# Kernel optimization log

Measured on AMD Instinct MI355X. Metric: run time of the kernel, lower is better.

## Reference

```python
import jax, jax.numpy as jnp
import numpy as np

B, N, C, H = 4, 1024, 1024, 16
HD = C // H
SCALE = HD ** -0.5


def _init_linear(key, out_dim, in_dim):
    # torch nn.Linear default init: U(-1/sqrt(in), 1/sqrt(in)) for weight and bias
    kw, kb = jax.random.split(key)
    bound = 1.0 / np.sqrt(in_dim)
    W = jax.random.uniform(kw, (out_dim, in_dim), jnp.float32, -bound, bound)
    b = jax.random.uniform(kb, (out_dim,), jnp.float32, -bound, bound)
    return W, b


def setup_inputs() -> dict:
    key = jax.random.key(0)
    ks = jax.random.split(key, 5)
    x = jax.random.normal(ks[0], (B, N, C), jnp.float32)
    # NdLinear qkv: Linear(N->N) along seq axis, then Linear(C->3C) along channel axis
    Wq0, bq0 = _init_linear(ks[1], N, N)
    Wq1, bq1 = _init_linear(ks[2], 3 * C, C)
    # NdLinear proj: Linear(N->N) along seq axis, then Linear(C->C) along channel axis
    Wp0, bp0 = _init_linear(ks[3], N, N)
    Wp1, bp1 = _init_linear(ks[4], C, C)
    return {"x": x, "Wq0": Wq0, "bq0": bq0, "Wq1": Wq1, "bq1": bq1,
            "Wp0": Wp0, "bp0": bp0, "Wp1": Wp1, "bp1": bp1}


def _ndlinear(x, W0, b0, W1, b1):
    # NdLinear over (seq, channel): apply Linear along axis 1, then axis 2.
    # torch Linear: y = x @ W.T + b
    x = jnp.einsum('bnc,mn->bmc', x, W0) + b0[None, :, None]   # seq axis
    x = jnp.einsum('bnc,dc->bnd', x, W1) + b1                  # channel axis
    return x


def reference(x, Wq0, bq0, Wq1, bq1, Wp0, bp0, Wp1, bp1):
    qkv = _ndlinear(x, Wq0, bq0, Wq1, bq1)                     # (B, N, 3C)
    qkv = qkv.reshape(B, N, 3, H, HD).transpose(2, 0, 3, 1, 4) # (3, B, H, N, HD)
    q, k, v = qkv[0], qkv[1], qkv[2]
    attn = jnp.einsum('bhnd,bhmd->bhnm', q, k) * SCALE         # (B, H, N, N)
    attn = jax.nn.softmax(attn, axis=-1)
    out = jnp.einsum('bhnm,bhmd->bhnd', attn, v)               # (B, H, N, HD)
    out = out.transpose(0, 2, 1, 3).reshape(B, N, C)
    out = _ndlinear(out, Wp0, bp0, Wp1, bp1)
    return out
```

## Files before the change

kernel.cpp:

```cpp
#include <hip/hip_runtime.h>
#include <hip/hip_bf16.h>
#include <stdint.h>

typedef __bf16 bf16;
typedef __bf16 bf16x4 __attribute__((ext_vector_type(4)));
typedef __bf16 bf16x8 __attribute__((ext_vector_type(8)));
typedef float f32x4 __attribute__((ext_vector_type(4)));

#define B_ 4
#define N_ 1024
#define C_ 1024
#define H_ 16
#define MEG (1u << 20)

__device__ __forceinline__ uint32_t lds_off(const void* p) {
    return (uint32_t)(uintptr_t)p;
}
__device__ __forceinline__ void g2l16(const void* g, uint32_t lds_byte) {
    __builtin_amdgcn_global_load_lds(
        (const __attribute__((address_space(1))) unsigned int*)(uintptr_t)g,
        (__attribute__((address_space(3))) unsigned int*)(uintptr_t)lds_byte,
        16, 0, 0);
}

__global__ __launch_bounds__(256) void cvt_k(const float* __restrict__ in,
                                             bf16* __restrict__ out, int n) {
    int i = (blockIdx.x * 256 + threadIdx.x) * 8;
    if (i >= n) return;
    float4 a = *(const float4*)(in + i);
    float4 b = *(const float4*)(in + i + 4);
    bf16x8 r;
    r[0] = (bf16)a.x; r[1] = (bf16)a.y; r[2] = (bf16)a.z; r[3] = (bf16)a.w;
    r[4] = (bf16)b.x; r[5] = (bf16)b.y; r[6] = (bf16)b.z; r[7] = (bf16)b.w;
    *(bf16x8*)(out + i) = r;
}

__global__ __launch_bounds__(256) void xpose_k(const float* __restrict__ x,
                                               bf16* __restrict__ xT) {
    __shared__ bf16 t[64][66];
    const int tid = threadIdx.x;
    const int b = blockIdx.z, n0 = blockIdx.y * 64, c0 = blockIdx.x * 64;
    {
        int nl = tid >> 2, seg = tid & 3;
        const float* src = x + ((size_t)b * N_ + n0 + nl) * C_ + c0 + seg * 16;
#pragma unroll
        for (int i = 0; i < 4; ++i) {
            float4 v = *(const float4*)(src + i * 4);
            t[nl][seg * 16 + i * 4 + 0] = (bf16)v.x;
            t[nl][seg * 16 + i * 4 + 1] = (bf16)v.y;
            t[nl][seg * 16 + i * 4 + 2] = (bf16)v.z;
            t[nl][seg * 16 + i * 4 + 3] = (bf16)v.w;
        }
    }
    __syncthreads();
    {
        int cl = tid >> 2, seg = tid & 3;
        bf16* dst = xT + ((size_t)b * C_ + c0 + cl) * N_ + n0 + seg * 16;
        bf16x8 o0, o1;
#pragma unroll
        for (int j = 0; j < 8; ++j) o0[j] = t[seg * 16 + j][cl];
#pragma unroll
        for (int j = 0; j < 8; ++j) o1[j] = t[seg * 16 + 8 + j][cl];
        *(bf16x8*)dst = o0;
        *(bf16x8*)(dst + 8) = o1;
    }
}

template <int BIAS, bool OF32>
__global__ __launch_bounds__(512) void gemm_k(
    const bf16* __restrict__ A, const bf16* __restrict__ Bm,
    const float* __restrict__ bias, void* __restrict__ Cv,
    int M, int Nn, int K, long long sA, long long sB, long long sC)
{
    __shared__ bf16 smem[2][2][128 * 64];

    const int tid = threadIdx.x;
    const int lane = tid & 63, wid = tid >> 6;
    const int lr = lane & 15, lg = lane >> 4;
    const int wr = wid >> 2, wc = wid & 3;
    const int m0 = blockIdx.y * 128, n0 = blockIdx.x * 128;

    const bf16* Ab = A + (size_t)blockIdx.z * sA;
    const bf16* Bb = Bm + (size_t)blockIdx.z * sB;

    const uint32_t a_lds0 = lds_off(&smem[0][0][0]);
    const uint32_t b_lds0 = lds_off(&smem[0][1][0]);
    const uint32_t bufstride = 2 * 128 * 64 * 2;

    auto stage = [&](int kt, int buf) {
#pragma unroll
        for (int half = 0; half < 2; ++half) {
            int it = tid + half * 512;
            int r = it >> 3, ch = it & 7;
            int sch = ch ^ (r & 7);
            g2l16(Ab + (size_t)(m0 + r) * K + kt * 64 + sch * 8,
                  a_lds0 + buf * bufstride + it * 16);
            g2l16(Bb + (size_t)(n0 + r) * K + kt * 64 + sch * 8,
                  b_lds0 + buf * bufstride + it * 16);
        }
    };

    f32x4 acc[4][2];
#pragma unroll
    for (int i = 0; i < 4; ++i)
#pragma unroll
        for (int j = 0; j < 2; ++j) { f32x4 z = {0.f,0.f,0.f,0.f}; acc[i][j] = z; }

    stage(0, 0);
    __syncthreads();

    const int nt = K >> 6;
    for (int t = 0; t < nt; ++t) {
        int buf = t & 1;
        if (t + 1 < nt) stage(t + 1, buf ^ 1);
        const bf16* As = &smem[buf][0][0];
        const bf16* Bs = &smem[buf][1][0];
#pragma unroll
        for (int s = 0; s < 2; ++s) {
            bf16x8 af[4], bfr[2];
#pragma unroll
            for (int mi = 0; mi < 4; ++mi) {
                int row = wr * 64 + mi * 16 + lr;
                int slot = (s * 4 + lg) ^ (row & 7);
                af[mi] = *(const bf16x8*)(As + row * 64 + slot * 8);
            }
#pragma unroll
            for (int ni = 0; ni < 2; ++ni) {
                int row = wc * 32 + ni * 16 + lr;
                int slot = (s * 4 + lg) ^ (row & 7);
                bfr[ni] = *(const bf16x8*)(Bs + row * 64 + slot * 8);
            }
#pragma unroll
            for (int mi = 0; mi < 4; ++mi)
#pragma unroll
                for (int ni = 0; ni < 2; ++ni)
                    acc[mi][ni] = __builtin_amdgcn_mfma_f32_16x16x32_bf16(
                        af[mi], bfr[ni], acc[mi][ni], 0, 0, 0);
        }
        __syncthreads();
    }

#pragma unroll
    for (int mi = 0; mi < 4; ++mi)
#pragma unroll
        for (int ni = 0; ni < 2; ++ni)
#pragma unroll
            for (int r = 0; r < 4; ++r) {
                int row = m0 + wr * 64 + mi * 16 + lg * 4 + r;
                int col = n0 + wc * 32 + ni * 16 + lr;
                float bv = (BIAS == 0) ? bias[row] : bias[col];
                float v = acc[mi][ni][r] + bv;
                if constexpr (OF32)
                    ((float*)Cv + (size_t)blockIdx.z * sC)[(size_t)row * Nn + col] = v;
                else
                    ((bf16*)Cv + (size_t)blockIdx.z * sC)[(size_t)row * Nn + col] = (bf16)v;
            }
}

__global__ __launch_bounds__(512) void attn_k(
    const bf16* __restrict__ qkv, bf16* __restrict__ aoT)
{
    __shared__ bf16 Ks[2][4096];
    __shared__ bf16 Vs[2][64][72];
    __shared__ bf16 pbuf[8][16][72];

    const int tid = threadIdx.x;
    const int lane = tid & 63, wid = tid >> 6;
    const int lr = lane & 15, lg = lane >> 4;
    const int bid = blockIdx.x;
    const int qt = bid >> 6, hb = bid & 63;
    const int b = hb >> 4, h = hb & 15;
    const int qrow0 = qt * 128 + wid * 16;
    const int hoff = h * 64;
    const bf16* qkvb = qkv + (size_t)b * (N_ * 3 * C_);

    bf16x8 qf[2];
#pragma unroll
    for (int kk = 0; kk < 2; ++kk)
        qf[kk] = *(const bf16x8*)(qkvb + (size_t)(qrow0 + lr) * 3072 +
                                  hoff + kk * 32 + lg * 8);

    const uint32_t ks0 = lds_off(&Ks[0][0]);
    const int vkey = tid >> 3, vdc = tid & 7;

    auto stageK = [&](int kt, int buf) {
        int key = tid >> 3, ch = tid & 7;
        int sch = ch ^ (key & 7);
        g2l16(qkvb + (size_t)(kt * 64 + key) * 3072 + C_ + hoff + sch * 8,
              ks0 + buf * 8192 + tid * 16);
    };
    auto loadV = [&](int kt) -> bf16x8 {
        return *(const bf16x8*)(qkvb + (size_t)(kt * 64 + vkey) * 3072 +
                                2 * C_ + hoff + vdc * 8);
    };
    auto writeV = [&](bf16x8 v, int buf) {
#pragma unroll
        for (int j = 0; j < 8; ++j) Vs[buf][vdc * 8 + j][vkey] = v[j];
    };

    float lsum[4] = {0.f, 0.f, 0.f, 0.f};
    f32x4 o[4];
#pragma unroll
    for (int i = 0; i < 4; ++i) { f32x4 z = {0.f,0.f,0.f,0.f}; o[i] = z; }

    stageK(0, 0);
    writeV(loadV(0), 0);
    __syncthreads();

    for (int kt = 0; kt < 16; ++kt) {
        int buf = kt & 1;
        bf16x8 vnext;
        if (kt + 1 < 16) {
            stageK(kt + 1, buf ^ 1);
            vnext = loadV(kt + 1);
        }

        f32x4 s[4];
#pragma unroll
        for (int st = 0; st < 4; ++st) {
            f32x4 z = {0.f, 0.f, 0.f, 0.f};
#pragma unroll
            for (int kk = 0; kk < 2; ++kk) {
                int row = st * 16 + lr;
                int slot = (kk * 4 + lg) ^ (row & 7);
                bf16x8 kf = *(const bf16x8*)(&Ks[buf][row * 64 + slot * 8]);
                z = __builtin_amdgcn_mfma_f32_16x16x32_bf16(qf[kk], kf, z, 0, 0, 0);
            }
            s[st] = z;
        }

#pragma unroll
        for (int st = 0; st < 4; ++st)
#pragma unroll
            for (int r = 0; r < 4; ++r) {
                float e = __expf(s[st][r] * 0.125f);
                bf16 pb = (bf16)e;
                lsum[r] += (float)pb;
                pbuf[wid][lg * 4 + r][st * 16 + lr] = pb;
            }

        bf16x8 pf[2];
        pf[0] = *(const bf16x8*)(&pbuf[wid][lr][lg * 8]);
        pf[1] = *(const bf16x8*)(&pbuf[wid][lr][32 + lg * 8]);

#pragma unroll
        for (int dt = 0; dt < 4; ++dt) {
            bf16x8 v0 = *(const bf16x8*)(&Vs[buf][dt * 16 + lr][lg * 8]);
            bf16x8 v1 = *(const bf16x8*)(&Vs[buf][dt * 16 + lr][32 + lg * 8]);
            o[dt] = __builtin_amdgcn_mfma_f32_16x16x32_bf16(pf[0], v0, o[dt], 0, 0, 0);
            o[dt] = __builtin_amdgcn_mfma_f32_16x16x32_bf16(pf[1], v1, o[dt], 0, 0, 0);
        }

        if (kt + 1 < 16) writeV(vnext, buf ^ 1);
        __syncthreads();
    }

#pragma unroll
    for (int m = 1; m < 16; m <<= 1)
#pragma unroll
        for (int r = 0; r < 4; ++r)
            lsum[r] += __shfl_xor(lsum[r], m, 64);

#pragma unroll
    for (int dt = 0; dt < 4; ++dt) {
        bf16x4 ov;
#pragma unroll
        for (int r = 0; r < 4; ++r) ov[r] = (bf16)(o[dt][r] / lsum[r]);
        size_t c = (size_t)b * C_ + hoff + dt * 16 + lr;
        *(bf16x4*)(aoT + c * N_ + qrow0 + lg * 4) = ov;
    }
}

extern "C" void kernel_launch(void* const* d_in, const int* in_sizes, int n_in,
                              void* d_out, int out_size, void* d_ws, size_t ws_size,
                              hipStream_t stream) {
    (void)in_sizes; (void)n_in; (void)out_size; (void)ws_size;
    const float* x   = (const float*)d_in[0];
    const float* Wq0 = (const float*)d_in[1];
    const float* bq0 = (const float*)d_in[2];
    const float* Wq1 = (const float*)d_in[3];
    const float* bq1 = (const float*)d_in[4];
    const float* Wp0 = (const float*)d_in[5];
    const float* bp0 = (const float*)d_in[6];
    const float* Wp1 = (const float*)d_in[7];
    const float* bp1 = (const float*)d_in[8];

    bf16* ws   = (bf16*)d_ws;
    bf16* xT   = ws;
    bf16* Wq0b = ws + 4 * MEG;
    bf16* Wq1b = ws + 5 * MEG;
    bf16* Wp0b = ws + 8 * MEG;
    bf16* Wp1b = ws + 9 * MEG;
    bf16* y1   = ws + 10 * MEG;
    bf16* y2   = ws + 14 * MEG;
    bf16* aoT  = y1;
    bf16* z1   = y2;
    float* outp = (float*)d_out;

    const long long s1M = (long long)N_ * C_;

    cvt_k<<<dim3(512), 256, 0, stream>>>(Wq0, Wq0b, 1 * MEG);
    cvt_k<<<dim3(1536), 256, 0, stream>>>(Wq1, Wq1b, 3 * MEG);
    cvt_k<<<dim3(512), 256, 0, stream>>>(Wp0, Wp0b, 1 * MEG);
    cvt_k<<<dim3(512), 256, 0, stream>>>(Wp1, Wp1b, 1 * MEG);
    xpose_k<<<dim3(16, 16, 4), 256, 0, stream>>>(x, xT);

    gemm_k<0, false><<<dim3(8, 8, 4), 512, 0, stream>>>(
        Wq0b, xT, bq0, y1, 1024, 1024, 1024, 0LL, s1M, s1M);
    gemm_k<1, false><<<dim3(24, 32, 1), 512, 0, stream>>>(
        y1, Wq1b, bq1, y2, 4096, 3072, 1024, 0LL, 0LL, 0LL);
    attn_k<<<dim3(512), 512, 0, stream>>>(y2, aoT);
    gemm_k<0, false><<<dim3(8, 8, 4), 512, 0, stream>>>(
        Wp0b, aoT, bp0, z1, 1024, 1024, 1024, 0LL, s1M, s1M);
    gemm_k<1, true><<<dim3(8, 32, 1), 512, 0, stream>>>(
        z1, Wp1b, bp1, outp, 4096, 1024, 1024, 0LL, 0LL, 0LL);
}
```

Before: 141.0 us.

## Merge weight conversion launches and swizzle transposed V tile in attention LDS

Combines the four fp32-to-bf16 weight conversion launches into a single kernel that selects its source by block index, cutting launch overhead. In the attention kernel, V is now transposed as it is gathered from global memory: each thread reads one dimension across 8 keys with strided scalar loads. It then writes a single 16-byte XOR-swizzled vector into a packed 64x64 LDS tile, replacing eight bank-conflicting scalar LDS stores per thread. The trade-off is less coalesced global loads for V, since there are 8 strided 2-byte reads per thread instead of one 16-byte read.

```diff
diff --git a/kernel.cpp b/kernel.cpp
--- a/kernel.cpp
+++ b/kernel.cpp
@@ -23,16 +23,24 @@
         16, 0, 0);
 }
 
-__global__ __launch_bounds__(256) void cvt_k(const float* __restrict__ in,
-                                             bf16* __restrict__ out, int n) {
-    int i = (blockIdx.x * 256 + threadIdx.x) * 8;
-    if (i >= n) return;
-    float4 a = *(const float4*)(in + i);
-    float4 b = *(const float4*)(in + i + 4);
+__global__ __launch_bounds__(256) void cvt4_k(
+    const float* __restrict__ s0, bf16* __restrict__ d0,
+    const float* __restrict__ s1, bf16* __restrict__ d1,
+    const float* __restrict__ s2, bf16* __restrict__ d2,
+    const float* __restrict__ s3, bf16* __restrict__ d3) {
+    int bid = blockIdx.x;
+    const float* s; bf16* d; int base;
+    if (bid < 512)       { s = s0; d = d0; base = 0; }
+    else if (bid < 2048) { s = s1; d = d1; base = 512; }
+    else if (bid < 2560) { s = s2; d = d2; base = 2048; }
+    else                 { s = s3; d = d3; base = 2560; }
+    int i = ((bid - base) * 256 + threadIdx.x) * 8;
+    float4 a = *(const float4*)(s + i);
+    float4 b = *(const float4*)(s + i + 4);
     bf16x8 r;
     r[0] = (bf16)a.x; r[1] = (bf16)a.y; r[2] = (bf16)a.z; r[3] = (bf16)a.w;
     r[4] = (bf16)b.x; r[5] = (bf16)b.y; r[6] = (bf16)b.z; r[7] = (bf16)b.w;
-    *(bf16x8*)(out + i) = r;
+    *(bf16x8*)(d + i) = r;
 }
 
 __global__ __launch_bounds__(256) void xpose_k(const float* __restrict__ x,
@@ -161,7 +169,7 @@
     const bf16* __restrict__ qkv, bf16* __restrict__ aoT)
 {
     __shared__ bf16 Ks[2][4096];
-    __shared__ bf16 Vs[2][64][72];
+    __shared__ bf16 Vs[2][4096];
     __shared__ bf16 pbuf[8][16][72];
 
     const int tid = threadIdx.x;
@@ -181,7 +189,7 @@
                                   hoff + kk * 32 + lg * 8);
 
     const uint32_t ks0 = lds_off(&Ks[0][0]);
-    const int vkey = tid >> 3, vdc = tid & 7;
+    const int vd = tid & 63, vkg = tid >> 6;
 
     auto stageK = [&](int kt, int buf) {
         int key = tid >> 3, ch = tid & 7;
@@ -190,12 +198,15 @@
               ks0 + buf * 8192 + tid * 16);
     };
     auto loadV = [&](int kt) -> bf16x8 {
-        return *(const bf16x8*)(qkvb + (size_t)(kt * 64 + vkey) * 3072 +
-                                2 * C_ + hoff + vdc * 8);
+        const bf16* base = qkvb + 2 * C_ + hoff + vd;
+        bf16x8 v;
+#pragma unroll
+        for (int j = 0; j < 8; ++j)
+            v[j] = base[(size_t)(kt * 64 + vkg * 8 + j) * 3072];
+        return v;
     };
     auto writeV = [&](bf16x8 v, int buf) {
-#pragma unroll
-        for (int j = 0; j < 8; ++j) Vs[buf][vdc * 8 + j][vkey] = v[j];
+        *(bf16x8*)(&Vs[buf][vd * 64 + ((vkg ^ (vd & 7)) * 8)]) = v;
     };
 
     float lsum[4] = {0.f, 0.f, 0.f, 0.f};
@@ -245,8 +256,9 @@
 
 #pragma unroll
         for (int dt = 0; dt < 4; ++dt) {
-            bf16x8 v0 = *(const bf16x8*)(&Vs[buf][dt * 16 + lr][lg * 8]);
-            bf16x8 v1 = *(const bf16x8*)(&Vs[buf][dt * 16 + lr][32 + lg * 8]);
+            int row = dt * 16 + lr;
+            bf16x8 v0 = *(const bf16x8*)(&Vs[buf][row * 64 + ((lg ^ (lr & 7)) * 8)]);
+            bf16x8 v1 = *(const bf16x8*)(&Vs[buf][row * 64 + (((4 + lg) ^ (lr & 7)) * 8)]);
             o[dt] = __builtin_amdgcn_mfma_f32_16x16x32_bf16(pf[0], v0, o[dt], 0, 0, 0);
             o[dt] = __builtin_amdgcn_mfma_f32_16x16x32_bf16(pf[1], v1, o[dt], 0, 0, 0);
         }
@@ -299,10 +311,8 @@
 
     const long long s1M = (long long)N_ * C_;
 
-    cvt_k<<<dim3(512), 256, 0, stream>>>(Wq0, Wq0b, 1 * MEG);
-    cvt_k<<<dim3(1536), 256, 0, stream>>>(Wq1, Wq1b, 3 * MEG);
-    cvt_k<<<dim3(512), 256, 0, stream>>>(Wp0, Wp0b, 1 * MEG);
-    cvt_k<<<dim3(512), 256, 0, stream>>>(Wp1, Wp1b, 1 * MEG);
+    cvt4_k<<<dim3(3072), 256, 0, stream>>>(Wq0, Wq0b, Wq1, Wq1b,
+                                           Wp0, Wp0b, Wp1, Wp1b);
     xpose_k<<<dim3(16, 16, 4), 256, 0, stream>>>(x, xT);
 
     gemm_k<0, false><<<dim3(8, 8, 4), 512, 0, stream>>>(
```

New measurement: 123.9 us. 12.1% less time.
